# Performance work log

Hardware: AMD Instinct MI355X
Metric: run time of the kernel (lower is better)

Reference implementation:

```python
import jax, jax.numpy as jnp
import numpy as np

SPARSITY = 0.01

def quantize(weight, s):
    # ternary quantization: (-s, 0, +s); computed under no_grad in torch
    pos = (weight > s).astype(weight.dtype)
    neg = (weight < -s).astype(weight.dtype)
    return (pos - neg) * s

def setup_inputs() -> dict:
    key = jax.random.key(0)
    k1, k2, k3 = jax.random.split(key, 3)
    B, N, Din, Dout = 8, 2048, 256, 256
    x = jax.random.normal(k1, (B, N, Din), dtype=jnp.float32)
    adj = jax.random.uniform(k2, (B, N, N), dtype=jnp.float32)
    # xavier_uniform_ over (in_dim, out_dim)
    limit = float(np.sqrt(6.0 / (Din + Dout)))
    weight = jax.random.uniform(k3, (Din, Dout), dtype=jnp.float32, minval=-limit, maxval=limit)
    bias = jnp.zeros((Dout,), dtype=jnp.float32)
    return {"x": x, "adj": adj, "weight": weight, "bias": bias}

def reference(x, adj, weight, bias):
    dw = quantize(weight, SPARSITY)          # [Din, Dout] ternary * s
    support = jnp.einsum('bni,io->bno', x, dw)   # [B, N, Dout]
    out = jnp.einsum('bnm,bmo->bno', adj, support) + bias
    return jax.nn.relu(out)
```

## Files before the change

kernel.cpp:

```cpp
#include <hip/hip_runtime.h>
#include <stdint.h>

typedef __attribute__((ext_vector_type(8))) short short8;
typedef __attribute__((ext_vector_type(4))) float f32x4;

static_assert(sizeof(short8) == 16, "frag size");

__device__ __forceinline__ uint16_t f2bf(float f) {
  uint32_t u = __builtin_bit_cast(uint32_t, f);
  u += 0x7fffu + ((u >> 16) & 1u);
  return (uint16_t)(u >> 16);
}

__device__ __forceinline__ void gload_lds16(const void* g, void* lds_wave_base) {
  __builtin_amdgcn_global_load_lds(
      (__attribute__((address_space(1))) void*)(void*)(g),
      (__attribute__((address_space(3))) void*)(lds_wave_base),
      16, 0, 0);
}


__global__ __launch_bounds__(256) void quant_kernel(const float* __restrict__ w,
                                                    uint16_t* __restrict__ dwT) {
  const int o = blockIdx.x, i = threadIdx.x;
  const float v = w[i * 256 + o];
  const float t = (v > 0.01f) ? 1.0f : ((v < -0.01f) ? -1.0f : 0.0f);
  dwT[o * 256 + (i ^ ((o & 7) << 3))] = f2bf(t);
}

#define SB_A 0
#define SB_B 16384

__global__ __launch_bounds__(256) void support_kernel(const float* __restrict__ x,
                                                      const uint16_t* __restrict__ dwT,
                                                      uint16_t* __restrict__ spt) {
  __shared__ __align__(16) unsigned char smem[24576];
  const int t = threadIdx.x, lane = t & 63, w = t >> 6;
  const int r = lane & 15, q = lane >> 4;
  const int g0 = (blockIdx.x & 127) * 128;
  const int o0 = (blockIdx.x >> 7) * 64;

  f32x4 acc[2][4] = {};

  for (int k0 = 0; k0 < 256; k0 += 64) {
#pragma unroll
    for (int it = 0; it < 4; ++it) {
      const int id = it * 256 + t, row = id >> 3, c = id & 7;
      const float* p = x + (size_t)(g0 + row) * 256 + k0 + c * 8;
      const float4 v0 = *(const float4*)p;
      const float4 v1 = *(const float4*)(p + 4);
      uint4 u;
      u.x = (uint32_t)f2bf(v0.x) | ((uint32_t)f2bf(v0.y) << 16);
      u.y = (uint32_t)f2bf(v0.z) | ((uint32_t)f2bf(v0.w) << 16);
      u.z = (uint32_t)f2bf(v1.x) | ((uint32_t)f2bf(v1.y) << 16);
      u.w = (uint32_t)f2bf(v1.z) | ((uint32_t)f2bf(v1.w) << 16);
      *(uint4*)(smem + SB_A + row * 128 + ((c ^ (row & 7)) << 4)) = u;
    }
#pragma unroll
    for (int j = 0; j < 2; ++j) {
      const int id = j * 256 + t, row = id >> 3, c = id & 7;
      gload_lds16(dwT + (size_t)(o0 + row) * 256 + k0 + c * 8,
                  smem + SB_B + (size_t)(j * 256 + w * 64) * 16);
    }
    __syncthreads();
#pragma unroll
    for (int h = 0; h < 2; ++h) {
      short8 av[2], bv[4];
      const int pc = (((h * 4 + q) ^ (r & 7)) << 4);
#pragma unroll
      for (int mi = 0; mi < 2; ++mi)
        av[mi] = *(const short8*)(smem + SB_A + (32 * w + 16 * mi + r) * 128 + pc);
#pragma unroll
      for (int ni = 0; ni < 4; ++ni)
        bv[ni] = *(const short8*)(smem + SB_B + (16 * ni + r) * 128 + pc);
#pragma unroll
      for (int mi = 0; mi < 2; ++mi)
#pragma unroll
        for (int ni = 0; ni < 4; ++ni)
          acc[mi][ni] = __builtin_amdgcn_mfma_f32_16x16x32_bf16(av[mi], bv[ni],
                                                                acc[mi][ni], 0, 0, 0);
    }
    __syncthreads();
  }
#pragma unroll
  for (int ni = 0; ni < 4; ++ni) {
    const int ol = 16 * ni + r;
#pragma unroll
    for (int mi = 0; mi < 2; ++mi)
#pragma unroll
      for (int reg = 0; reg < 4; ++reg) {
        const int gl = 32 * w + 16 * mi + 4 * q + reg;
        const int gsw = gl ^ ((ol & 7) << 3);
        *(uint16_t*)(smem + (ol * 128 + gsw) * 2) = f2bf(acc[mi][ni][reg] * 0.01f);
      }
  }
  __syncthreads();
#pragma unroll
  for (int it = 0; it < 4; ++it) {
    const int id = it * 256 + t, row = id >> 4, cc = id & 15;
    const uint4 u = *(const uint4*)(smem + (row * 128 + cc * 8) * 2);
    *(uint4*)(spt + (size_t)(o0 + row) * 16384 + g0 + cc * 8) = u;
  }
}

#define MB_A 0
#define MB_B 4096

__global__ __launch_bounds__(256) void gcn_main_kernel(const float* __restrict__ adj,
                                                       const uint16_t* __restrict__ spt,
                                                       const float* __restrict__ bias,
                                                       float* __restrict__ out) {
  __shared__ __align__(16) unsigned char smem[36864];
  const int t = threadIdx.x, lane = t & 63, w = t >> 6;
  const int r = lane & 15, q = lane >> 4;
  const int bb = blockIdx.x & 7;
  const int n0 = (blockIdx.x >> 3) * 32;
  const float* adjb = adj + ((size_t)bb * 2048 + n0) * 2048;
  const uint16_t* sptb = spt + (size_t)bb * 2048;

  f32x4 acc[2][4] = {};

  for (int k0 = 0; k0 < 2048; k0 += 64) {
    {
      const int row = t >> 3, c = t & 7;
      const float* p = adjb + (size_t)row * 2048 + k0 + c * 8;
      const float4 v0 = *(const float4*)p;
      const float4 v1 = *(const float4*)(p + 4);
      uint4 u;
      u.x = (uint32_t)f2bf(v0.x) | ((uint32_t)f2bf(v0.y) << 16);
      u.y = (uint32_t)f2bf(v0.z) | ((uint32_t)f2bf(v0.w) << 16);
      u.z = (uint32_t)f2bf(v1.x) | ((uint32_t)f2bf(v1.y) << 16);
      u.w = (uint32_t)f2bf(v1.z) | ((uint32_t)f2bf(v1.w) << 16);
      *(uint4*)(smem + MB_A + row * 128 + ((c ^ (row & 7)) << 4)) = u;
    }
#pragma unroll
    for (int j = 0; j < 8; ++j) {
      const int id = j * 256 + t, row = id >> 3, c = id & 7;
      gload_lds16(sptb + (size_t)row * 16384 + k0 + c * 8,
                  smem + MB_B + (size_t)(j * 256 + w * 64) * 16);
    }
    __syncthreads();
#pragma unroll
    for (int h = 0; h < 2; ++h) {
      short8 av[2], bv[4];
      const int pc = (((h * 4 + q) ^ (r & 7)) << 4);
#pragma unroll
      for (int mi = 0; mi < 2; ++mi)
        av[mi] = *(const short8*)(smem + MB_A + (16 * mi + r) * 128 + pc);
#pragma unroll
      for (int ni = 0; ni < 4; ++ni)
        bv[ni] = *(const short8*)(smem + MB_B + (w * 64 + 16 * ni + r) * 128 + pc);
#pragma unroll
      for (int mi = 0; mi < 2; ++mi)
#pragma unroll
        for (int ni = 0; ni < 4; ++ni)
          acc[mi][ni] = __builtin_amdgcn_mfma_f32_16x16x32_bf16(av[mi], bv[ni],
                                                                acc[mi][ni], 0, 0, 0);
    }
    __syncthreads();
  }
#pragma unroll
  for (int ni = 0; ni < 4; ++ni) {
    const int o = w * 64 + 16 * ni + r;
    const float bs = bias[o];
#pragma unroll
    for (int mi = 0; mi < 2; ++mi)
#pragma unroll
      for (int reg = 0; reg < 4; ++reg) {
        const int n = n0 + 16 * mi + 4 * q + reg;
        out[((size_t)bb * 2048 + n) * 256 + o] = fmaxf(acc[mi][ni][reg] + bs, 0.0f);
      }
  }
}

extern "C" void kernel_launch(void* const* d_in, const int* in_sizes, int n_in,
                              void* d_out, int out_size, void* d_ws, size_t ws_size,
                              hipStream_t stream) {
  const float* x      = (const float*)d_in[0];
  const float* adj    = (const float*)d_in[1];
  const float* weight = (const float*)d_in[2];
  const float* bias   = (const float*)d_in[3];
  float* out = (float*)d_out;

  uint16_t* dwT = (uint16_t*)d_ws;
  uint16_t* spt = (uint16_t*)((char*)d_ws + 131072);

  hipLaunchKernelGGL(quant_kernel,    dim3(256), dim3(256), 0, stream, weight, dwT);
  hipLaunchKernelGGL(support_kernel,  dim3(512), dim3(256), 0, stream, x, dwT, spt);
  hipLaunchKernelGGL(gcn_main_kernel, dim3(512), dim3(256), 0, stream, adj, spt, bias, out);
}
```

Before: 236.3 us.

## Double-buffer LDS in GCN main kernel to prefetch next adj/support tile

Splits the shared-memory staging in the adjacency-times-support kernel into two buffers. The loads for tile k+1 (the async support loads straight into LDS and the adj float loads into registers) are issued before the MFMA work on tile k, and the converted adj tile is written into the other buffer afterwards. This hides global-load latency behind compute and drops one barrier per iteration. In exchange the LDS footprint doubles to 72 KB, which can lower occupancy, and register pressure rises from holding the prefetched values.

```diff
diff --git a/kernel.cpp b/kernel.cpp
--- a/kernel.cpp
+++ b/kernel.cpp
@@ -103,14 +103,13 @@
   }
 }
 
-#define MB_A 0
-#define MB_B 4096
+#define MBUF 36864
 
 __global__ __launch_bounds__(256) void gcn_main_kernel(const float* __restrict__ adj,
                                                        const uint16_t* __restrict__ spt,
                                                        const float* __restrict__ bias,
                                                        float* __restrict__ out) {
-  __shared__ __align__(16) unsigned char smem[36864];
+  __shared__ __align__(16) unsigned char smem[2 * MBUF];
   const int t = threadIdx.x, lane = t & 63, w = t >> 6;
   const int r = lane & 15, q = lane >> 4;
   const int bb = blockIdx.x & 7;
@@ -118,47 +117,77 @@
   const float* adjb = adj + ((size_t)bb * 2048 + n0) * 2048;
   const uint16_t* sptb = spt + (size_t)bb * 2048;
 
+  const int arow = t >> 3, ac = t & 7;
+  const float* aptr = adjb + (size_t)arow * 2048 + ac * 8;
+  const int aoff = arow * 128 + ((ac ^ (arow & 7)) << 4);
+
   f32x4 acc[2][4] = {};
 
-  for (int k0 = 0; k0 < 2048; k0 += 64) {
-    {
-      const int row = t >> 3, c = t & 7;
-      const float* p = adjb + (size_t)row * 2048 + k0 + c * 8;
-      const float4 v0 = *(const float4*)p;
-      const float4 v1 = *(const float4*)(p + 4);
+  {
+#pragma unroll
+    for (int j = 0; j < 8; ++j) {
+      const int id = j * 256 + t, row = id >> 3, c = id & 7;
+      gload_lds16(sptb + (size_t)row * 16384 + c * 8,
+                  smem + 4096 + (size_t)(j * 256 + w * 64) * 16);
+    }
+    const float4 v0 = *(const float4*)(aptr);
+    const float4 v1 = *(const float4*)(aptr + 4);
+    uint4 u;
+    u.x = (uint32_t)f2bf(v0.x) | ((uint32_t)f2bf(v0.y) << 16);
+    u.y = (uint32_t)f2bf(v0.z) | ((uint32_t)f2bf(v0.w) << 16);
+    u.z = (uint32_t)f2bf(v1.x) | ((uint32_t)f2bf(v1.y) << 16);
+    u.w = (uint32_t)f2bf(v1.z) | ((uint32_t)f2bf(v1.w) << 16);
+    *(uint4*)(smem + aoff) = u;
+  }
+
+  for (int k = 0; k < 32; ++k) {
+    const int p = k & 1;
+    unsigned char* cur = smem + p * MBUF;
+    unsigned char* nxt = smem + (p ^ 1) * MBUF;
+    __syncthreads();
+
+    float4 v0, v1;
+    const bool pf = (k + 1) < 32;
+    if (pf) {
+      const int k1 = (k + 1) * 64;
+#pragma unroll
+      for (int j = 0; j < 8; ++j) {
+        const int id = j * 256 + t, row = id >> 3, c = id & 7;
+        gload_lds16(sptb + (size_t)row * 16384 + k1 + c * 8,
+                    nxt + 4096 + (size_t)(j * 256 + w * 64) * 16);
+      }
+      v0 = *(const float4*)(aptr + k1);
+      v1 = *(const float4*)(aptr + k1 + 4);
+    }
+
+#pragma unroll
+    for (int h = 0; h < 2; ++h) {
+      short8 av[2], bv[4];
+      const int pc = (((h * 4 + q) ^ (r & 7)) << 4);
+#pragma unroll
+      for (int mi = 0; mi < 2; ++mi)
+        av[mi] = *(const short8*)(cur + (16 * mi + r) * 128 + pc);
+#pragma unroll
+      for (int ni = 0; ni < 4; ++ni)
+        bv[ni] = *(const short8*)(cur + 4096 + (w * 64 + 16 * ni + r) * 128 + pc);
+#pragma unroll
+      for (int mi = 0; mi < 2; ++mi)
+#pragma unroll
+        for (int ni = 0; ni < 4; ++ni)
+          acc[mi][ni] = __builtin_amdgcn_mfma_f32_16x16x32_bf16(av[mi], bv[ni],
+                                                                acc[mi][ni], 0, 0, 0);
+    }
+
+    if (pf) {
       uint4 u;
       u.x = (uint32_t)f2bf(v0.x) | ((uint32_t)f2bf(v0.y) << 16);
       u.y = (uint32_t)f2bf(v0.z) | ((uint32_t)f2bf(v0.w) << 16);
       u.z = (uint32_t)f2bf(v1.x) | ((uint32_t)f2bf(v1.y) << 16);
       u.w = (uint32_t)f2bf(v1.z) | ((uint32_t)f2bf(v1.w) << 16);
-      *(uint4*)(smem + MB_A + row * 128 + ((c ^ (row & 7)) << 4)) = u;
-    }
-#pragma unroll
-    for (int j = 0; j < 8; ++j) {
-      const int id = j * 256 + t, row = id >> 3, c = id & 7;
-      gload_lds16(sptb + (size_t)row * 16384 + k0 + c * 8,
-                  smem + MB_B + (size_t)(j * 256 + w * 64) * 16);
-    }
-    __syncthreads();
-#pragma unroll
-    for (int h = 0; h < 2; ++h) {
-      short8 av[2], bv[4];
-      const int pc = (((h * 4 + q) ^ (r & 7)) << 4);
-#pragma unroll
-      for (int mi = 0; mi < 2; ++mi)
-        av[mi] = *(const short8*)(smem + MB_A + (16 * mi + r) * 128 + pc);
-#pragma unroll
-      for (int ni = 0; ni < 4; ++ni)
-        bv[ni] = *(const short8*)(smem + MB_B + (w * 64 + 16 * ni + r) * 128 + pc);
-#pragma unroll
-      for (int mi = 0; mi < 2; ++mi)
-#pragma unroll
-        for (int ni = 0; ni < 4; ++ni)
-          acc[mi][ni] = __builtin_amdgcn_mfma_f32_16x16x32_bf16(av[mi], bv[ni],
-                                                                acc[mi][ni], 0, 0, 0);
-    }
-    __syncthreads();
-  }
+      *(uint4*)(nxt + aoff) = u;
+    }
+  }
+
 #pragma unroll
   for (int ni = 0; ni < 4; ++ni) {
     const int o = w * 64 + 16 * ni + r;
```

Measured after the change: 239.6 us. Within noise of the previous version (+1.4%).
